# Kernel optimization log

Measured on AMD Instinct MI355X. Metric: run time of the kernel, lower is better.

The kernel has to match this reference:

```python
import jax, jax.numpy as jnp
import numpy as np

N, S_CT, D = 64, 128, 1024
WIN = 5
EPS = 1e-8
STOP = 0.1
MAX_DEPTH = 25


def layer_norm(x, g, b, eps=1e-5):
    mu = jnp.mean(x, axis=-1, keepdims=True)
    var = jnp.var(x, axis=-1, keepdims=True)
    return (x - mu) / jnp.sqrt(var + eps) * g + b


def _augment(sequence, input_mask, START, END):
    n, s, d = sequence.shape
    seq = jnp.concatenate([jnp.broadcast_to(START, (n, 1, d)), sequence], axis=1)
    m = jnp.concatenate([jnp.ones((n, 1, 1), seq.dtype), input_mask], axis=1)
    m_no_end = jnp.concatenate([m, jnp.zeros((n, 1, 1), seq.dtype)], axis=1)
    m_yes_end = jnp.concatenate([jnp.ones((n, 1, 1), seq.dtype), m], axis=1)
    end_mask = m_yes_end - m_no_end  # one-hot at END slot
    seq = jnp.concatenate([seq, jnp.zeros((n, 1, d), seq.dtype)], axis=1)
    seq = end_mask * END + (1.0 - end_mask) * seq
    m_no_start = jnp.concatenate([jnp.zeros((n, 1, 1), seq.dtype), m_yes_end[:, 1:]], axis=1)
    return seq, m_yes_end, end_mask, m_no_start, m_no_end


def _neighbor_probs(exist_probs, mask):
    # exist_probs, mask: (n,s,1). Returns left/right soft-neighbor matrices (n,s,s).
    n, s, _ = mask.shape
    m = jnp.stack([mask[:, ::-1, 0], mask[:, :, 0]], axis=1)            # (n,2,s)
    p = jnp.stack([exist_probs[:, ::-1, 0], exist_probs[:, :, 0]], axis=1)
    tri = jnp.triu(jnp.ones((s, s), mask.dtype), k=1)
    mat = (p * m)[:, :, None, :] * tri                                   # (n,2,s,s)
    cs = jnp.cumsum(mat, axis=-1)
    rem_left = jnp.concatenate([jnp.ones((n, 2, s, 1), mask.dtype), 1.0 - cs[..., :-1]], axis=-1)
    rem_left = jnp.maximum(rem_left, 0.0)
    right = jnp.where(cs > 1.0, rem_left, mat) * m[:, :, None, :]
    left = jnp.flip(right[:, 0], axis=(1, 2))
    return left, right[:, 1]


def crvnn_forward(sequence, input_mask, START, END, W_conv, b_conv, W_scorer, b_scorer,
                  W_init, b_init, W_cell1, b_cell1, W_cell2, b_cell2,
                  ln1_g, ln1_b, ln2_g, ln2_b):
    seq, mask, end_mask, m_no_start, m_no_end = _augment(sequence, input_mask, START, END)
    n, s, d = seq.shape
    last_mask = jnp.concatenate([end_mask[:, 1:], jnp.zeros((n, 1, 1), seq.dtype)], axis=1)
    sel_mask = m_no_start * m_no_end * (1.0 - last_mask)  # start_end_last_mask
    seq = layer_norm((seq * mask) @ W_init + b_init, ln1_g, ln1_b) * mask
    exist = jnp.ones((n, s, 1), seq.dtype) * mask

    def step(carry, _):
        sq, ep, um = carry
        L, R = _neighbor_probs(ep, mask)
        l1 = L @ sq; l2 = L @ l1
        r1 = R @ sq; r2 = R @ r1
        win = jnp.concatenate([l2, l1, sq, r1, r2], axis=-1)  # (n,s,5d) == stacked window flattened
        h = jax.nn.gelu(win @ W_conv + b_conv, approximate=False)
        sc = h @ W_scorer + b_scorer                           # (n,s,1) transition score
        scores = jnp.concatenate([sc, jnp.zeros_like(sc)], axis=-1)
        exp_scores = jnp.exp(scores - jnp.max(scores))
        exp_t = exp_scores[..., 0:1] * sel_mask
        exp_n = exp_scores[..., 1:2]
        # sum_normalize over {transition, no_op}; gate halted samples via um (tp=0 => no-op)
        tp = exp_t / (exp_t + exp_n + 2.0 * EPS) * um[:, None, None]
        # compose(left_child, self)
        cat = jnp.concatenate([l1, sq], axis=-1)
        hid = jax.nn.gelu(cat @ W_cell1 + b_cell1, approximate=False)
        contents = (hid @ W_cell2 + b_cell2).reshape(n, s, 4, d)
        gates = jax.nn.sigmoid(contents[:, :, 0:3, :])
        comp = layer_norm(gates[:, :, 0] * l1 + gates[:, :, 1] * sq + gates[:, :, 2] * contents[:, :, 3, :], ln2_g, ln2_b)
        new_sq = tp * comp + (1.0 - tp) * sq
        new_ep = ep * (1.0 - (R @ tp))  # left neighbor consumed with prob of right neighbor transition
        active = jnp.sum(new_ep * sel_mask, axis=(1, 2))
        new_um = um * (active >= STOP).astype(sq.dtype)
        return (new_sq, new_ep, new_um), None

    steps = min(s - 2, MAX_DEPTH)
    (seq, exist, _), _ = jax.lax.scan(step, (seq, exist, jnp.ones((n,), seq.dtype)), None, length=steps)
    seq = seq * mask
    global_state = jnp.sum(last_mask * seq, axis=1)  # root lands at last content slot
    return seq[:, 1:-1, :], global_state


def setup_inputs():
    key = jax.random.key(0)
    ks = jax.random.split(key, 8)
    sc = 0.02
    f32 = jnp.float32
    return {
        "sequence": jax.random.normal(ks[0], (N, S_CT, D), f32),
        "input_mask": jnp.ones((N, S_CT, 1), f32),
        "START": jax.random.normal(ks[1], (D,), f32),
        "END": jax.random.normal(ks[2], (D,), f32),
        "W_conv": jax.random.normal(ks[3], (WIN * D, D), f32) * sc,
        "b_conv": jnp.zeros((D,), f32),
        "W_scorer": jax.random.normal(ks[4], (D, 1), f32) * sc,
        "b_scorer": jnp.zeros((1,), f32),
        "W_init": jax.random.normal(ks[5], (D, D), f32) * sc,
        "b_init": jnp.zeros((D,), f32),
        "W_cell1": jax.random.normal(ks[6], (2 * D, 4 * D), f32) * sc,
        "b_cell1": jnp.zeros((4 * D,), f32),
        "W_cell2": jax.random.normal(ks[7], (4 * D, 4 * D), f32) * sc,
        "b_cell2": jnp.zeros((4 * D,), f32),
        "ln1_g": jnp.ones((D,), f32), "ln1_b": jnp.zeros((D,), f32),
        "ln2_g": jnp.ones((D,), f32), "ln2_b": jnp.zeros((D,), f32),
    }


def reference(sequence, input_mask, START, END, W_conv, b_conv, W_scorer, b_scorer,
              W_init, b_init, W_cell1, b_cell1, W_cell2, b_cell2,
              ln1_g, ln1_b, ln2_g, ln2_b):
    return crvnn_forward(sequence, input_mask, START, END, W_conv, b_conv, W_scorer, b_scorer,
                         W_init, b_init, W_cell1, b_cell1, W_cell2, b_cell2,
                         ln1_g, ln1_b, ln2_g, ln2_b)
```

## Files before the change

kernel.cpp:

```cpp
#include <hip/hip_runtime.h>
#include <math.h>


#define NB 64
#define SS 130
#define DD 1024
#define MM (NB*SS)
#define LSTR 132
#define CROWS 1664

typedef _Float16 f16x8 __attribute__((ext_vector_type(8)));
typedef _Float16 f16x4 __attribute__((ext_vector_type(4)));
typedef _Float16 f16x2 __attribute__((ext_vector_type(2)));
typedef float f32x4 __attribute__((ext_vector_type(4)));

struct GemmSrc { const float* a[5]; };

__device__ __forceinline__ float bsum(float v){
  __shared__ float sh[4];
  __syncthreads();
  #pragma unroll
  for (int o=32;o;o>>=1) v += __shfl_down(v,o);
  if ((threadIdx.x & 63)==0) sh[threadIdx.x>>6] = v;
  __syncthreads();
  return sh[0]+sh[1]+sh[2]+sh[3];
}
__device__ __forceinline__ float bmaxr(float v){
  __shared__ float sh[4];
  __syncthreads();
  #pragma unroll
  for (int o=32;o;o>>=1) v = fmaxf(v,__shfl_down(v,o));
  if ((threadIdx.x & 63)==0) sh[threadIdx.x>>6] = v;
  __syncthreads();
  return fmaxf(fmaxf(sh[0],sh[1]),fmaxf(sh[2],sh[3]));
}
__device__ __forceinline__ float gelu_(float x){
  return 0.5f*x*(1.f+erff(x*0.70710678118654752f));
}

__global__ __launch_bounds__(256) void build_masks(
    const float* __restrict__ im, float* __restrict__ mk, float* __restrict__ sel,
    float* __restrict__ lastm, float* __restrict__ endm, float* __restrict__ ep,
    float* __restrict__ um, int* __restrict__ flag){
  int b = blockIdx.x, i = threadIdx.x;
  if (i < SS){
    float mye = (i<=1) ? 1.f : im[b*128 + (i-2)];
    float mne = (i==SS-1) ? 0.f : ((i==0) ? 1.f : im[b*128 + (i-1)]);
    float em  = mye - mne;
    float mns = (i==0) ? 0.f : mye;
    float lm;
    if (i < SS-1){
      int i1 = i+1;
      float mye1 = (i1<=1) ? 1.f : im[b*128 + (i1-2)];
      float mne1 = (i1==SS-1) ? 0.f : im[b*128 + (i1-1)];
      lm = mye1 - mne1;
    } else lm = 0.f;
    float sl = mns * mne * (1.f - lm);
    int idx = b*SS + i;
    mk[idx]=mye; sel[idx]=sl; lastm[idx]=lm; endm[idx]=em; ep[idx]=mye;
  } else if (i == SS) { um[b] = 1.f; }
  else if (i == SS+1 && b==0) { flag[0] = 0; }
}

__global__ __launch_bounds__(256) void build_seq(
    const float* __restrict__ seqin, const float* __restrict__ START,
    const float* __restrict__ END, const float* __restrict__ mk,
    const float* __restrict__ endm, float* __restrict__ out){
  int r = blockIdx.x; int b = r/SS, i = r%SS; int t = threadIdx.x;
  float em = endm[r], m = mk[r];
  #pragma unroll
  for (int q=0;q<4;q++){
    int j = t + q*256;
    float v;
    if (i==0) v = START[j];
    else if (i<=128) v = seqin[((size_t)b*128 + (i-1))*DD + j];
    else v = 0.f;
    v = em*END[j] + (1.f-em)*v;
    out[(size_t)r*DD + j] = v*m;
  }
}

__global__ __launch_bounds__(256) void wtranspose(
    const float* __restrict__ W, _Float16* __restrict__ WTh, _Float16* __restrict__ WTl,
    int K, int N){
  __shared__ float Ts[32][33];
  int k0 = blockIdx.x*32, n0 = blockIdx.y*32;
  int t = threadIdx.x;
  int r = t>>3, c4 = (t&7)*4;
  float4 v = *(const float4*)(W + (size_t)(k0+r)*N + n0 + c4);
  Ts[r][c4]=v.x; Ts[r][c4+1]=v.y; Ts[r][c4+2]=v.z; Ts[r][c4+3]=v.w;
  __syncthreads();
  int n = t>>3, k4 = (t&7)*4;
  f16x4 h, lo;
  #pragma unroll
  for (int i=0;i<4;i++){
    float xs = Ts[k4+i][n] * 64.f;
    _Float16 hh = (_Float16)xs;
    h[i] = hh; lo[i] = (_Float16)((xs - (float)hh) * 2048.f);
  }
  *(f16x4*)(WTh + (size_t)(n0+n)*K + k0+k4) = h;
  *(f16x4*)(WTl + (size_t)(n0+n)*K + k0+k4) = lo;
}

template<bool PRE>
__global__ __launch_bounds__(256,2) void gemm_mfma(
    GemmSrc S, long lda,
    const _Float16* __restrict__ WTh, const _Float16* __restrict__ WTl,
    const float* __restrict__ Wf, int Nw,
    const float* __restrict__ bias,
    float* __restrict__ C, long ldc, int K, int act,
    const int* __restrict__ flag, float* __restrict__ spart, const float* __restrict__ Ws){
  if (flag[0]) return;
  __shared__ _Float16 Ah[128][40], Al[128][40];
  __shared__ _Float16 Wh[128][40], Wl[128][40];
  const int t = threadIdx.x;
  const int wave = t >> 6, lane = t & 63;
  const int wm = wave >> 1, wn = wave & 1;
  const int l15 = lane & 15, l4 = lane >> 4;
  const long mb = (long)blockIdx.y * 128;
  const int  nb = blockIdx.x * 128;
  f32x4 accH[4][4], accX[4][4];
  #pragma unroll
  for (int i=0;i<4;i++)
    #pragma unroll
    for (int j=0;j<4;j++){ accH[i][j] = (f32x4){0.f,0.f,0.f,0.f}; accX[i][j] = (f32x4){0.f,0.f,0.f,0.f}; }

  for (int kt=0; kt<K; kt+=32){
    #pragma unroll
    for (int p=0;p<4;p++){
      int f = t + 256*p;
      int m = f >> 3;
      int k4 = (f & 7) * 4;
      int kg = kt + k4;
      const float* src = S.a[kg >> 10];
      float4 v = *(const float4*)(src + (mb + m)*lda + (kg & 1023));
      f16x4 h, lo;
      _Float16 hh;
      hh=(_Float16)v.x; h[0]=hh; lo[0]=(_Float16)((v.x-(float)hh)*2048.f);
      hh=(_Float16)v.y; h[1]=hh; lo[1]=(_Float16)((v.y-(float)hh)*2048.f);
      hh=(_Float16)v.z; h[2]=hh; lo[2]=(_Float16)((v.z-(float)hh)*2048.f);
      hh=(_Float16)v.w; h[3]=hh; lo[3]=(_Float16)((v.w-(float)hh)*2048.f);
      *(f16x4*)&Ah[m][k4] = h;
      *(f16x4*)&Al[m][k4] = lo;
    }
    if constexpr (PRE){
      #pragma unroll
      for (int p=0;p<2;p++){
        int f = t + 256*p;
        int n = f >> 2;
        int ko = (f & 3) * 8;
        *(f16x8*)&Wh[n][ko] = *(const f16x8*)(WTh + (size_t)(nb + n)*K + kt + ko);
        *(f16x8*)&Wl[n][ko] = *(const f16x8*)(WTl + (size_t)(nb + n)*K + kt + ko);
      }
    } else {
      #pragma unroll
      for (int p=0;p<2;p++){
        int u = t + 256*p;
        int kp = u >> 5;
        int c  = u & 31;
        const float* wsrc = Wf + (size_t)(kt + 2*kp)*Nw + nb + c;
        #pragma unroll
        for (int i=0;i<4;i++){
          float x0 = wsrc[32*i] * 64.f;
          float x1 = wsrc[(size_t)Nw + 32*i] * 64.f;
          _Float16 h0 = (_Float16)x0, h1 = (_Float16)x1;
          _Float16 g0 = (_Float16)((x0 - (float)h0)*2048.f);
          _Float16 g1 = (_Float16)((x1 - (float)h1)*2048.f);
          f16x2 hp; hp[0]=h0; hp[1]=h1;
          f16x2 lp; lp[0]=g0; lp[1]=g1;
          int n = c + 32*i;
          *(f16x2*)&Wh[n][2*kp] = hp;
          *(f16x2*)&Wl[n][2*kp] = lp;
        }
      }
    }
    __syncthreads();
    f16x8 wh[4], wl[4];
    #pragma unroll
    for (int i=0;i<4;i++){
      wh[i] = *(const f16x8*)&Wh[wn*64 + i*16 + l15][8*l4];
      wl[i] = *(const f16x8*)&Wl[wn*64 + i*16 + l15][8*l4];
    }
    #pragma unroll
    for (int mi=0;mi<4;mi++){
      f16x8 ahv = *(const f16x8*)&Ah[wm*64 + mi*16 + l15][8*l4];
      f16x8 alv = *(const f16x8*)&Al[wm*64 + mi*16 + l15][8*l4];
      #pragma unroll
      for (int ni=0;ni<4;ni++){
        accH[mi][ni] = __builtin_amdgcn_mfma_f32_16x16x32_f16(wh[ni], ahv, accH[mi][ni], 0,0,0);
        accX[mi][ni] = __builtin_amdgcn_mfma_f32_16x16x32_f16(wh[ni], alv, accX[mi][ni], 0,0,0);
        accX[mi][ni] = __builtin_amdgcn_mfma_f32_16x16x32_f16(wl[ni], ahv, accX[mi][ni], 0,0,0);
      }
    }
    __syncthreads();
  }

  const float IH = 1.f/64.f, IX = 1.f/131072.f;
  if (act==2){
    #pragma unroll
    for (int mi=0;mi<4;mi++){
      float s = 0.f;
      #pragma unroll
      for (int ni=0;ni<4;ni++){
        int nbase = nb + wn*64 + ni*16 + 4*l4;
        #pragma unroll
        for (int r=0;r<4;r++){
          float v = gelu_(accH[mi][ni][r]*IH + accX[mi][ni][r]*IX + bias[nbase+r]);
          s = fmaf(v, Ws[nbase+r], s);
        }
      }
      s += __shfl_xor(s, 16);
      s += __shfl_xor(s, 32);
      if (l4==0){
        long m = mb + wm*64 + mi*16 + l15;
        spart[m*16 + blockIdx.x*2 + wn] = s;
      }
    }
    return;
  }
  #pragma unroll
  for (int mi=0;mi<4;mi++){
    long m = mb + wm*64 + mi*16 + l15;
    #pragma unroll
    for (int ni=0;ni<4;ni++){
      int nbase = nb + wn*64 + ni*16 + 4*l4;
      float4 v;
      v.x = accH[mi][ni][0]*IH + accX[mi][ni][0]*IX + bias[nbase+0];
      v.y = accH[mi][ni][1]*IH + accX[mi][ni][1]*IX + bias[nbase+1];
      v.z = accH[mi][ni][2]*IH + accX[mi][ni][2]*IX + bias[nbase+2];
      v.w = accH[mi][ni][3]*IH + accX[mi][ni][3]*IX + bias[nbase+3];
      if (act==1){ v.x=gelu_(v.x); v.y=gelu_(v.y); v.z=gelu_(v.z); v.w=gelu_(v.w); }
      *(float4*)(C + m*ldc + nbase) = v;
    }
  }
}

__global__ __launch_bounds__(256,2) void gemm_f32(
    GemmSrc S, long lda, const float* __restrict__ B, const float* __restrict__ bias,
    float* __restrict__ C, long ldc, int N, int K, int act,
    const int* __restrict__ flag){
  if (flag[0]) return;
  __shared__ float Asm[16][132];
  __shared__ float Bsm[16][132];
  float acc[8][8];
  #pragma unroll
  for (int i=0;i<8;i++)
    #pragma unroll
    for (int j=0;j<8;j++) acc[i][j]=0.f;
  const int t = threadIdx.x;
  const int tx = t & 15, ty = t >> 4;
  const long mb = (long)blockIdx.y * 128;
  const int  nb = blockIdx.x * 128;
  for (int kt=0; kt<K; kt+=16){
    #pragma unroll
    for (int ii=0; ii<2; ii++){
      int f  = t + 256*ii;
      int m  = f >> 2;
      int k4 = (f & 3) * 4;
      int kg = kt + k4;
      const float* src = S.a[kg >> 10];
      float4 v = *(const float4*)(src + (mb + m)*lda + (kg & 1023));
      Asm[k4+0][m]=v.x; Asm[k4+1][m]=v.y; Asm[k4+2][m]=v.z; Asm[k4+3][m]=v.w;
    }
    #pragma unroll
    for (int ii=0; ii<2; ii++){
      int f  = t + 256*ii;
      int kk = f >> 5;
      int c4 = (f & 31)*4;
      *(float4*)&Bsm[kk][c4] = *(const float4*)(B + (long)(kt+kk)*N + nb + c4);
    }
    __syncthreads();
    #pragma unroll
    for (int kk=0;kk<16;kk++){
      float av[8], bv[8];
      *(float4*)&av[0] = *(const float4*)&Asm[kk][ty*4];
      *(float4*)&av[4] = *(const float4*)&Asm[kk][64+ty*4];
      *(float4*)&bv[0] = *(const float4*)&Bsm[kk][tx*4];
      *(float4*)&bv[4] = *(const float4*)&Bsm[kk][64+tx*4];
      #pragma unroll
      for (int r=0;r<8;r++)
        #pragma unroll
        for (int c=0;c<8;c++) acc[r][c] = fmaf(av[r],bv[c],acc[r][c]);
    }
    __syncthreads();
  }
  #pragma unroll
  for (int rh=0;rh<2;rh++)
  #pragma unroll
  for (int rr=0;rr<4;rr++){
    long row = mb + rh*64 + ty*4 + rr;
    #pragma unroll
    for (int ch=0;ch<2;ch++){
      int col = nb + ch*64 + tx*4;
      float t0 = acc[rh*4+rr][ch*4+0] + bias[col+0];
      float t1 = acc[rh*4+rr][ch*4+1] + bias[col+1];
      float t2 = acc[rh*4+rr][ch*4+2] + bias[col+2];
      float t3 = acc[rh*4+rr][ch*4+3] + bias[col+3];
      if (act==1){ t0=gelu_(t0); t1=gelu_(t1); t2=gelu_(t2); t3=gelu_(t3); }
      float4 v; v.x=t0; v.y=t1; v.z=t2; v.w=t3;
      *(float4*)(C + row*ldc + col) = v;
    }
  }
}

__global__ __launch_bounds__(256,2) void bgemm(
    const float* __restrict__ P, const float* __restrict__ X, float* __restrict__ Y,
    const int* __restrict__ flag){
  if (flag[0]) return;
  __shared__ float Ps[64][17];
  __shared__ float Xs[16][132];
  const int t = threadIdx.x;
  const int nt = blockIdx.x, mt = blockIdx.y, b = blockIdx.z;
  const int i0 = mt*64;
  const float* Pb = P + (size_t)b*SS*LSTR;
  const float* Xb = X + (size_t)b*SS*DD + nt*128;
  float* Yb = Y + (size_t)b*SS*DD + nt*128;
  const int tx = t & 7, ty = t >> 3;
  float acc[2][16];
  #pragma unroll
  for (int r=0;r<2;r++)
    #pragma unroll
    for (int c=0;c<16;c++) acc[r][c]=0.f;
  for (int j0=0;j0<SS;j0+=16){
    { int r = t>>2, c0 = (t&3)*4;
      float4 v = make_float4(0.f,0.f,0.f,0.f);
      if (i0 + r < SS && j0 + c0 < LSTR) v = *(const float4*)(Pb + (size_t)(i0+r)*LSTR + j0 + c0);
      Ps[r][c0]=v.x; Ps[r][c0+1]=v.y; Ps[r][c0+2]=v.z; Ps[r][c0+3]=v.w;
    }
    #pragma unroll
    for (int ii=0;ii<2;ii++){
      int f = t + 256*ii;
      int jj = f>>5, c4 = (f&31)*4;
      float4 v = make_float4(0.f,0.f,0.f,0.f);
      if (j0 + jj < SS) v = *(const float4*)(Xb + (size_t)(j0+jj)*DD + c4);
      *(float4*)&Xs[jj][c4] = v;
    }
    __syncthreads();
    #pragma unroll
    for (int jj=0;jj<16;jj++){
      float p0 = Ps[2*ty][jj], p1 = Ps[2*ty+1][jj];
      #pragma unroll
      for (int q=0;q<4;q++){
        float4 xv = *(const float4*)&Xs[jj][tx*4 + 32*q];
        acc[0][q*4+0] = fmaf(p0,xv.x,acc[0][q*4+0]);
        acc[0][q*4+1] = fmaf(p0,xv.y,acc[0][q*4+1]);
        acc[0][q*4+2] = fmaf(p0,xv.z,acc[0][q*4+2]);
        acc[0][q*4+3] = fmaf(p0,xv.w,acc[0][q*4+3]);
        acc[1][q*4+0] = fmaf(p1,xv.x,acc[1][q*4+0]);
        acc[1][q*4+1] = fmaf(p1,xv.y,acc[1][q*4+1]);
        acc[1][q*4+2] = fmaf(p1,xv.z,acc[1][q*4+2]);
        acc[1][q*4+3] = fmaf(p1,xv.w,acc[1][q*4+3]);
      }
    }
    __syncthreads();
  }
  #pragma unroll
  for (int rr=0;rr<2;rr++){
    int row = i0 + 2*ty + rr;
    if (row < SS){
      #pragma unroll
      for (int q=0;q<4;q++){
        float4 v = make_float4(acc[rr][q*4],acc[rr][q*4+1],acc[rr][q*4+2],acc[rr][q*4+3]);
        *(float4*)(Yb + (size_t)row*DD + tx*4 + 32*q) = v;
      }
    }
  }
}

__global__ void neighbor_kernel(const float* __restrict__ ep, const float* __restrict__ mk,
                                float* __restrict__ L, float* __restrict__ R,
                                const int* __restrict__ flag){
  if (flag[0]) return;
  int idx = blockIdx.x*blockDim.x + threadIdx.x;
  if (idx >= MM) return;
  int b = idx / SS, i = idx % SS;
  const float* p = ep + b*SS;
  const float* m = mk + b*SS;
  float* Lr = L + (size_t)idx*LSTR;
  float* Rr = R + (size_t)idx*LSTR;
  for (int j=0;j<LSTR;j++){ Lr[j]=0.f; Rr[j]=0.f; }
  float cs=0.f;
  for (int j=i+1;j<SS;j++){
    float mat = p[j]*m[j];
    cs += mat;
    float v = (cs>1.f) ? fmaxf(1.f-(cs-mat),0.f) : mat;
    Rr[j] = v*m[j];
  }
  cs=0.f;
  for (int j=i-1;j>=0;j--){
    float mat = p[j]*m[j];
    cs += mat;
    float v = (cs>1.f) ? fmaxf(1.f-(cs-mat),0.f) : mat;
    Lr[j] = v*m[j];
  }
}

__global__ __launch_bounds__(256) void ln1_kernel(
    const float* __restrict__ xin, const float* __restrict__ g, const float* __restrict__ bb,
    const float* __restrict__ mk, float* __restrict__ out){
  int r = blockIdx.x, t = threadIdx.x;
  const float* xr = xin + (size_t)r*DD;
  float x[4]; float s=0.f;
  #pragma unroll
  for (int q=0;q<4;q++){ x[q]=xr[t+256*q]; s+=x[q]; }
  float mean = bsum(s)*(1.f/DD);
  float vs=0.f;
  #pragma unroll
  for (int q=0;q<4;q++){ float d=x[q]-mean; vs+=d*d; }
  float var = bsum(vs)*(1.f/DD);
  float inv = 1.f/sqrtf(var+1e-5f);
  float m = mk[r];
  #pragma unroll
  for (int q=0;q<4;q++){ int j=t+256*q; out[(size_t)r*DD+j] = ((x[q]-mean)*inv*g[j]+bb[j])*m; }
}

__global__ void scorer_final(const float* __restrict__ spart, const float* __restrict__ bs,
                             float* __restrict__ sc, const int* __restrict__ flag){
  if (flag[0]) return;
  int r = blockIdx.x*blockDim.x + threadIdx.x;
  if (r >= MM) return;
  float s = bs[0];
  #pragma unroll
  for (int k=0;k<16;k++) s += spart[(size_t)r*16+k];
  sc[r] = s;
}
__global__ __launch_bounds__(256) void max1(const float* __restrict__ sc, float* __restrict__ part,
                                            const int* __restrict__ flag){
  if (flag[0]) return;
  int idx = blockIdx.x*256 + threadIdx.x;
  float v = -1e30f;
  for (int i = idx; i < MM; i += 64*256) v = fmaxf(v, sc[i]);
  v = bmaxr(v);
  if (threadIdx.x==0) part[blockIdx.x] = v;
}
__global__ __launch_bounds__(64) void max2(const float* __restrict__ part, float* __restrict__ gm,
                                           const int* __restrict__ flag){
  if (flag[0]) return;
  float v = part[threadIdx.x];
  #pragma unroll
  for (int o=32;o;o>>=1) v = fmaxf(v, __shfl_down(v,o));
  if (threadIdx.x==0) gm[0] = fmaxf(v, 0.f);
}
__global__ void tp_kernel(const float* __restrict__ sc, const float* __restrict__ sel,
                          const float* __restrict__ um, const float* __restrict__ gm,
                          float* __restrict__ tp, const int* __restrict__ flag){
  if (flag[0]) return;
  int idx = blockIdx.x*blockDim.x + threadIdx.x;
  if (idx>=MM) return;
  int b = idx / SS;
  float g = gm[0];
  float et = expf(sc[idx]-g)*sel[idx];
  float en = expf(-g);
  tp[idx] = et/(et+en+2e-8f)*um[b];
}

__global__ __launch_bounds__(256) void update_kernel(
    const float* __restrict__ cont, const float* __restrict__ l1, float* __restrict__ sq,
    const float* __restrict__ tp, const float* __restrict__ g, const float* __restrict__ bb,
    const int* __restrict__ flag, long row0){
  if (flag[0]) return;
  long r = row0 + blockIdx.x; int t = threadIdx.x;
  const float* cr = cont + (size_t)blockIdx.x*4096;
  const float* lr = l1 + (size_t)r*DD;
  float* sr = sq + (size_t)r*DD;
  float x[4], sv[4];
  float s=0.f;
  #pragma unroll
  for (int q=0;q<4;q++){
    int j = t+q*256;
    float c0=cr[j], c1=cr[DD+j], c2=cr[2*DD+j], c3=cr[3*DD+j];
    float g0=1.f/(1.f+expf(-c0));
    float g1=1.f/(1.f+expf(-c1));
    float g2=1.f/(1.f+expf(-c2));
    float lv=lr[j]; float sqv=sr[j]; sv[q]=sqv;
    x[q] = g0*lv + g1*sqv + g2*c3;
    s += x[q];
  }
  float mean = bsum(s)*(1.f/DD);
  float vs=0.f;
  #pragma unroll
  for (int q=0;q<4;q++){ float d=x[q]-mean; vs+=d*d; }
  float var = bsum(vs)*(1.f/DD);
  float inv = 1.f/sqrtf(var+1e-5f);
  float tpv = tp[r];
  #pragma unroll
  for (int q=0;q<4;q++){
    int j=t+q*256;
    float comp = (x[q]-mean)*inv*g[j]+bb[j];
    sr[j] = tpv*comp + (1.f-tpv)*sv[q];
  }
}

__global__ void ep_update(float* __restrict__ ep, const float* __restrict__ R,
                          const float* __restrict__ tp, const int* __restrict__ flag){
  if (flag[0]) return;
  int idx = blockIdx.x*blockDim.x + threadIdx.x;
  if (idx>=MM) return;
  int b = idx / SS;
  const float* Rr = R + (size_t)idx*LSTR;
  const float* tb = tp + b*SS;
  float d=0.f;
  for (int j=0;j<SS;j++) d = fmaf(Rr[j],tb[j],d);
  ep[idx] *= (1.f - d);
}
__global__ __launch_bounds__(256) void active_um(const float* __restrict__ ep,
                                                 const float* __restrict__ sel,
                                                 float* __restrict__ um,
                                                 const int* __restrict__ flag){
  if (flag[0]) return;
  int b = blockIdx.x, t = threadIdx.x;
  float s = (t<SS) ? ep[b*SS+t]*sel[b*SS+t] : 0.f;
  s = bsum(s);
  if (t==0) um[b] *= (s >= 0.1f) ? 1.f : 0.f;
}
__global__ __launch_bounds__(64) void done_kernel(const float* __restrict__ um, int* __restrict__ flag){
  float v = um[threadIdx.x];
  unsigned long long b = __ballot(v > 0.f);
  if (threadIdx.x==0) flag[0] = (b==0ULL) ? 1 : 0;
}

__global__ __launch_bounds__(256) void output_kernel(const float* __restrict__ sq,
                                                     const float* __restrict__ mk,
                                                     float* __restrict__ out){
  int r = blockIdx.x; int b = r/SS, i = r%SS;
  if (i<1 || i>128) return;
  float m = mk[r]; int t=threadIdx.x;
  #pragma unroll
  for (int q=0;q<4;q++){
    int j = t+q*256;
    out[((size_t)b*128 + (i-1))*DD + j] = sq[(size_t)r*DD + j]*m;
  }
}
__global__ __launch_bounds__(256) void gstate_kernel(const float* __restrict__ sq,
                                                     const float* __restrict__ mk,
                                                     const float* __restrict__ lastm,
                                                     float* __restrict__ outg){
  int b = blockIdx.x; int t=threadIdx.x;
  #pragma unroll
  for (int q=0;q<4;q++){
    int j = t+q*256;
    float acc=0.f;
    for (int i=0;i<SS;i++){
      float w = lastm[b*SS+i]*mk[b*SS+i];
      acc = fmaf(w, sq[((size_t)(b*SS+i))*DD + j], acc);
    }
    outg[(size_t)b*DD + j] = acc;
  }
}

extern "C" void kernel_launch(void* const* d_in, const int* in_sizes, int n_in,
                              void* d_out, int out_size, void* d_ws, size_t ws_size,
                              hipStream_t stream) {
  const float* sequence   = (const float*)d_in[0];
  const float* input_mask = (const float*)d_in[1];
  const float* START      = (const float*)d_in[2];
  const float* END        = (const float*)d_in[3];
  const float* W_conv     = (const float*)d_in[4];
  const float* b_conv     = (const float*)d_in[5];
  const float* W_scorer   = (const float*)d_in[6];
  const float* b_scorer   = (const float*)d_in[7];
  const float* W_init     = (const float*)d_in[8];
  const float* b_init     = (const float*)d_in[9];
  const float* W_cell1    = (const float*)d_in[10];
  const float* b_cell1    = (const float*)d_in[11];
  const float* W_cell2    = (const float*)d_in[12];
  const float* b_cell2    = (const float*)d_in[13];
  const float* ln1g       = (const float*)d_in[14];
  const float* ln1b       = (const float*)d_in[15];
  const float* ln2g       = (const float*)d_in[16];
  const float* ln2b       = (const float*)d_in[17];

  float* ws = (float*)d_ws;
  const size_t U = (size_t)MM*DD;
  float* sq   = ws;
  float* l1   = ws + U;
  float* r1   = ws + 2*U;
  float* l2   = ws + 3*U;
  float* r2   = ws + 4*U;
  float* Lm   = ws + 5*U;
  float* Rm   = Lm + (size_t)NB*SS*LSTR;
  float* maskv= Rm + (size_t)NB*SS*LSTR;
  float* sel  = maskv + MM;
  float* lastm= sel + MM;
  float* endm = lastm + MM;
  float* ep   = endm + MM;
  float* scb  = ep + MM;
  float* tpb  = scb + MM;
  float* spart= tpb + MM;
  float* umb  = spart + (size_t)MM*16;
  float* part = umb + NB;
  float* gmx  = part + 64;
  int*   flag = (int*)(gmx + 4);
  size_t used_floats = (size_t)((float*)(flag+4) - ws);
  used_floats = (used_floats + 7) & ~(size_t)7;
  _Float16* WTc_h = (_Float16*)(ws + used_floats);
  const size_t SC = (size_t)1024*5120, S1 = (size_t)4096*2048, S2 = (size_t)4096*4096;
  _Float16* WTc_l = WTc_h + SC;
  _Float16* WT1_h = WTc_l + SC;
  _Float16* WT1_l = WT1_h + S1;
  _Float16* WT2_h = WT1_l + S1;
  _Float16* WT2_l = WT2_h + S2;
  size_t need_pre = (size_t)((char*)(WT2_l + S2) - (char*)d_ws);
  const bool pre = ws_size >= need_pre;

  build_masks<<<NB,256,0,stream>>>(input_mask, maskv, sel, lastm, endm, ep, umb, flag);
  build_seq<<<MM,256,0,stream>>>(sequence, START, END, maskv, endm, r1);
  GemmSrc si; si.a[0]=r1; si.a[1]=r1; si.a[2]=r1; si.a[3]=r1; si.a[4]=r1;
  gemm_f32<<<dim3(8,65),256,0,stream>>>(si, DD, W_init, b_init, l2, DD, DD, DD, 0, flag);
  ln1_kernel<<<MM,256,0,stream>>>(l2, ln1g, ln1b, maskv, sq);

  if (pre){
    wtranspose<<<dim3(160,32),256,0,stream>>>(W_conv,  WTc_h, WTc_l, 5120, 1024);
    wtranspose<<<dim3(64,128),256,0,stream>>>(W_cell1, WT1_h, WT1_l, 2048, 4096);
    wtranspose<<<dim3(128,128),256,0,stream>>>(W_cell2, WT2_h, WT2_l, 4096, 4096);
  }

  for (int it=0; it<25; ++it){
    neighbor_kernel<<<(MM+255)/256,256,0,stream>>>(ep, maskv, Lm, Rm, flag);
    bgemm<<<dim3(8,3,NB),256,0,stream>>>(Lm, sq, l1, flag);
    bgemm<<<dim3(8,3,NB),256,0,stream>>>(Rm, sq, r1, flag);
    bgemm<<<dim3(8,3,NB),256,0,stream>>>(Lm, l1, l2, flag);
    bgemm<<<dim3(8,3,NB),256,0,stream>>>(Rm, r1, r2, flag);
    GemmSrc s5; s5.a[0]=l2; s5.a[1]=l1; s5.a[2]=sq; s5.a[3]=r1; s5.a[4]=r2;
    if (pre)
      gemm_mfma<true ><<<dim3(8,65),256,0,stream>>>(s5, DD, WTc_h, WTc_l, nullptr, 0, b_conv, nullptr, 0, 5120, 2, flag, spart, W_scorer);
    else
      gemm_mfma<false><<<dim3(8,65),256,0,stream>>>(s5, DD, nullptr, nullptr, W_conv, 1024, b_conv, nullptr, 0, 5120, 2, flag, spart, W_scorer);
    scorer_final<<<(MM+255)/256,256,0,stream>>>(spart, b_scorer, scb, flag);
    max1<<<64,256,0,stream>>>(scb, part, flag);
    max2<<<1,64,0,stream>>>(part, gmx, flag);
    tp_kernel<<<(MM+255)/256,256,0,stream>>>(scb, sel, umb, gmx, tpb, flag);
    for (int c=0;c<5;c++){
      long row0 = (long)c*CROWS;
      GemmSrc s2; s2.a[0]=l1+row0*DD; s2.a[1]=sq+row0*DD; s2.a[2]=s2.a[1]; s2.a[3]=s2.a[1]; s2.a[4]=s2.a[1];
      GemmSrc s3; s3.a[0]=l2; s3.a[1]=l2+DD; s3.a[2]=l2+2*DD; s3.a[3]=l2+3*DD; s3.a[4]=l2;
      if (pre){
        gemm_mfma<true ><<<dim3(32,13),256,0,stream>>>(s2, DD,   WT1_h, WT1_l, nullptr, 0, b_cell1, l2, 4096, 2048, 1, flag, nullptr, nullptr);
        gemm_mfma<true ><<<dim3(32,13),256,0,stream>>>(s3, 4096, WT2_h, WT2_l, nullptr, 0, b_cell2, r2, 4096, 4096, 0, flag, nullptr, nullptr);
      } else {
        gemm_mfma<false><<<dim3(32,13),256,0,stream>>>(s2, DD,   nullptr, nullptr, W_cell1, 4096, b_cell1, l2, 4096, 2048, 1, flag, nullptr, nullptr);
        gemm_mfma<false><<<dim3(32,13),256,0,stream>>>(s3, 4096, nullptr, nullptr, W_cell2, 4096, b_cell2, r2, 4096, 4096, 0, flag, nullptr, nullptr);
      }
      update_kernel<<<CROWS,256,0,stream>>>(r2, l1, sq, tpb, ln2g, ln2b, flag, row0);
    }
    ep_update<<<(MM+255)/256,256,0,stream>>>(ep, Rm, tpb, flag);
    active_um<<<NB,256,0,stream>>>(ep, sel, umb, flag);
    done_kernel<<<1,64,0,stream>>>(umb, flag);
  }

  float* out = (float*)d_out;
  output_kernel<<<MM,256,0,stream>>>(sq, maskv, out);
  gstate_kernel<<<NB,256,0,stream>>>(sq, maskv, lastm, out + (size_t)NB*128*DD);
}
```

Measured before the change: 68.64 ms.

## Widen MFMA GEMM tiles to 128x256 with 512 threads and XCD-aware block remap

```diff
diff --git a/kernel.cpp b/kernel.cpp
--- a/kernel.cpp
+++ b/kernel.cpp
@@ -103,7 +103,7 @@
 }
 
 template<bool PRE>
-__global__ __launch_bounds__(256,2) void gemm_mfma(
+__global__ __launch_bounds__(512,2) void gemm_mfma(
     GemmSrc S, long lda,
     const _Float16* __restrict__ WTh, const _Float16* __restrict__ WTl,
     const float* __restrict__ Wf, int Nw,
@@ -112,13 +112,20 @@
     const int* __restrict__ flag, float* __restrict__ spart, const float* __restrict__ Ws){
   if (flag[0]) return;
   __shared__ _Float16 Ah[128][40], Al[128][40];
-  __shared__ _Float16 Wh[128][40], Wl[128][40];
+  __shared__ _Float16 Wh[256][40], Wl[256][40];
   const int t = threadIdx.x;
   const int wave = t >> 6, lane = t & 63;
-  const int wm = wave >> 1, wn = wave & 1;
+  const int wm = wave >> 2, wn = wave & 3;
   const int l15 = lane & 15, l4 = lane >> 4;
-  const long mb = (long)blockIdx.y * 128;
-  const int  nb = blockIdx.x * 128;
+  int lin = blockIdx.y * gridDim.x + blockIdx.x;
+  int nwg = gridDim.x * gridDim.y;
+  int q = nwg >> 3, r = nwg & 7;
+  int xcd = lin & 7, pos = lin >> 3;
+  int wg = (xcd < r) ? (xcd*(q+1) + pos) : (r*(q+1) + (xcd - r)*q + pos);
+  int MT = gridDim.y;
+  int mt = wg % MT, nt = wg / MT;
+  const long mb = (long)mt * 128;
+  const int  nb = nt * 256;
   f32x4 accH[4][4], accX[4][4];
   #pragma unroll
   for (int i=0;i<4;i++)
@@ -127,8 +134,8 @@
 
   for (int kt=0; kt<K; kt+=32){
     #pragma unroll
-    for (int p=0;p<4;p++){
-      int f = t + 256*p;
+    for (int p=0;p<2;p++){
+      int f = t + 512*p;
       int m = f >> 3;
       int k4 = (f & 7) * 4;
       int kg = kt + k4;
@@ -146,32 +153,28 @@
     if constexpr (PRE){
       #pragma unroll
       for (int p=0;p<2;p++){
-        int f = t + 256*p;
+        int f = t + 512*p;
         int n = f >> 2;
         int ko = (f & 3) * 8;
         *(f16x8*)&Wh[n][ko] = *(const f16x8*)(WTh + (size_t)(nb + n)*K + kt + ko);
         *(f16x8*)&Wl[n][ko] = *(const f16x8*)(WTl + (size_t)(nb + n)*K + kt + ko);
       }
     } else {
+      int kp = t >> 5;
+      int c  = t & 31;
+      const float* wsrc = Wf + (size_t)(kt + 2*kp)*Nw + nb + c;
       #pragma unroll
-      for (int p=0;p<2;p++){
-        int u = t + 256*p;
-        int kp = u >> 5;
-        int c  = u & 31;
-        const float* wsrc = Wf + (size_t)(kt + 2*kp)*Nw + nb + c;
-        #pragma unroll
-        for (int i=0;i<4;i++){
-          float x0 = wsrc[32*i] * 64.f;
-          float x1 = wsrc[(size_t)Nw + 32*i] * 64.f;
-          _Float16 h0 = (_Float16)x0, h1 = (_Float16)x1;
-          _Float16 g0 = (_Float16)((x0 - (float)h0)*2048.f);
-          _Float16 g1 = (_Float16)((x1 - (float)h1)*2048.f);
-          f16x2 hp; hp[0]=h0; hp[1]=h1;
-          f16x2 lp; lp[0]=g0; lp[1]=g1;
-          int n = c + 32*i;
-          *(f16x2*)&Wh[n][2*kp] = hp;
-          *(f16x2*)&Wl[n][2*kp] = lp;
-        }
+      for (int i=0;i<8;i++){
+        float x0 = wsrc[32*i] * 64.f;
+        float x1 = wsrc[(size_t)Nw + 32*i] * 64.f;
+        _Float16 h0 = (_Float16)x0, h1 = (_Float16)x1;
+        _Float16 g0 = (_Float16)((x0 - (float)h0)*2048.f);
+        _Float16 g1 = (_Float16)((x1 - (float)h1)*2048.f);
+        f16x2 hp; hp[0]=h0; hp[1]=h1;
+        f16x2 lp; lp[0]=g0; lp[1]=g1;
+        int n = c + 32*i;
+        *(f16x2*)&Wh[n][2*kp] = hp;
+        *(f16x2*)&Wl[n][2*kp] = lp;
       }
     }
     __syncthreads();
@@ -204,16 +207,16 @@
       for (int ni=0;ni<4;ni++){
         int nbase = nb + wn*64 + ni*16 + 4*l4;
         #pragma unroll
-        for (int r=0;r<4;r++){
-          float v = gelu_(accH[mi][ni][r]*IH + accX[mi][ni][r]*IX + bias[nbase+r]);
-          s = fmaf(v, Ws[nbase+r], s);
+        for (int rr=0;rr<4;rr++){
+          float v = gelu_(accH[mi][ni][rr]*IH + accX[mi][ni][rr]*IX + bias[nbase+rr]);
+          s = fmaf(v, Ws[nbase+rr], s);
         }
       }
       s += __shfl_xor(s, 16);
       s += __shfl_xor(s, 32);
       if (l4==0){
         long m = mb + wm*64 + mi*16 + l15;
-        spart[m*16 + blockIdx.x*2 + wn] = s;
+        spart[m*16 + nt*4 + wn] = s;
       }
     }
     return;
@@ -593,15 +596,16 @@
   int*   flag = (int*)(gmx + 4);
   size_t used_floats = (size_t)((float*)(flag+4) - ws);
   used_floats = (used_floats + 7) & ~(size_t)7;
-  _Float16* WTc_h = (_Float16*)(ws + used_floats);
   const size_t SC = (size_t)1024*5120, S1 = (size_t)4096*2048, S2 = (size_t)4096*4096;
+  _Float16* WT2_h = (_Float16*)(ws + used_floats);
+  _Float16* WT2_l = WT2_h + S2;
+  _Float16* WT1_h = WT2_l + S2;
+  _Float16* WT1_l = WT1_h + S1;
+  _Float16* WTc_h = WT1_l + S1;
   _Float16* WTc_l = WTc_h + SC;
-  _Float16* WT1_h = WTc_l + SC;
-  _Float16* WT1_l = WT1_h + S1;
-  _Float16* WT2_h = WT1_l + S1;
-  _Float16* WT2_l = WT2_h + S2;
-  size_t need_pre = (size_t)((char*)(WT2_l + S2) - (char*)d_ws);
-  const bool pre = ws_size >= need_pre;
+  const bool pre2 = ws_size >= (size_t)((char*)(WT2_l + S2) - (char*)d_ws);
+  const bool pre1 = ws_size >= (size_t)((char*)(WT1_l + S1) - (char*)d_ws);
+  const bool prec = ws_size >= (size_t)((char*)(WTc_l + SC) - (char*)d_ws);
 
   build_masks<<<NB,256,0,stream>>>(input_mask, maskv, sel, lastm, endm, ep, umb, flag);
   build_seq<<<MM,256,0,stream>>>(sequence, START, END, maskv, endm, r1);
@@ -609,11 +613,9 @@
   gemm_f32<<<dim3(8,65),256,0,stream>>>(si, DD, W_init, b_init, l2, DD, DD, DD, 0, flag);
   ln1_kernel<<<MM,256,0,stream>>>(l2, ln1g, ln1b, maskv, sq);
 
-  if (pre){
-    wtranspose<<<dim3(160,32),256,0,stream>>>(W_conv,  WTc_h, WTc_l, 5120, 1024);
-    wtranspose<<<dim3(64,128),256,0,stream>>>(W_cell1, WT1_h, WT1_l, 2048, 4096);
-    wtranspose<<<dim3(128,128),256,0,stream>>>(W_cell2, WT2_h, WT2_l, 4096, 4096);
-  }
+  if (pre2) wtranspose<<<dim3(128,128),256,0,stream>>>(W_cell2, WT2_h, WT2_l, 4096, 4096);
+  if (pre1) wtranspose<<<dim3(64,128),256,0,stream>>>(W_cell1, WT1_h, WT1_l, 2048, 4096);
+  if (prec) wtranspose<<<dim3(160,32),256,0,stream>>>(W_conv,  WTc_h, WTc_l, 5120, 1024);
 
   for (int it=0; it<25; ++it){
     neighbor_kernel<<<(MM+255)/256,256,0,stream>>>(ep, maskv, Lm, Rm, flag);
@@ -622,10 +624,10 @@
     bgemm<<<dim3(8,3,NB),256,0,stream>>>(Lm, l1, l2, flag);
     bgemm<<<dim3(8,3,NB),256,0,stream>>>(Rm, r1, r2, flag);
     GemmSrc s5; s5.a[0]=l2; s5.a[1]=l1; s5.a[2]=sq; s5.a[3]=r1; s5.a[4]=r2;
-    if (pre)
-      gemm_mfma<true ><<<dim3(8,65),256,0,stream>>>(s5, DD, WTc_h, WTc_l, nullptr, 0, b_conv, nullptr, 0, 5120, 2, flag, spart, W_scorer);
+    if (prec)
+      gemm_mfma<true ><<<dim3(4,65),512,0,stream>>>(s5, DD, WTc_h, WTc_l, nullptr, 0, b_conv, nullptr, 0, 5120, 2, flag, spart, W_scorer);
     else
-      gemm_mfma<false><<<dim3(8,65),256,0,stream>>>(s5, DD, nullptr, nullptr, W_conv, 1024, b_conv, nullptr, 0, 5120, 2, flag, spart, W_scorer);
+      gemm_mfma<false><<<dim3(4,65),512,0,stream>>>(s5, DD, nullptr, nullptr, W_conv, 1024, b_conv, nullptr, 0, 5120, 2, flag, spart, W_scorer);
     scorer_final<<<(MM+255)/256,256,0,stream>>>(spart, b_scorer, scb, flag);
     max1<<<64,256,0,stream>>>(scb, part, flag);
     max2<<<1,64,0,stream>>>(part, gmx, flag);
@@ -634,13 +636,14 @@
       long row0 = (long)c*CROWS;
       GemmSrc s2; s2.a[0]=l1+row0*DD; s2.a[1]=sq+row0*DD; s2.a[2]=s2.a[1]; s2.a[3]=s2.a[1]; s2.a[4]=s2.a[1];
       GemmSrc s3; s3.a[0]=l2; s3.a[1]=l2+DD; s3.a[2]=l2+2*DD; s3.a[3]=l2+3*DD; s3.a[4]=l2;
-      if (pre){
-        gemm_mfma<true ><<<dim3(32,13),256,0,stream>>>(s2, DD,   WT1_h, WT1_l, nullptr, 0, b_cell1, l2, 4096, 2048, 1, flag, nullptr, nullptr);
-        gemm_mfma<true ><<<dim3(32,13),256,0,stream>>>(s3, 4096, WT2_h, WT2_l, nullptr, 0, b_cell2, r2, 4096, 4096, 0, flag, nullptr, nullptr);
-      } else {
-        gemm_mfma<false><<<dim3(32,13),256,0,stream>>>(s2, DD,   nullptr, nullptr, W_cell1, 4096, b_cell1, l2, 4096, 2048, 1, flag, nullptr, nullptr);
-        gemm_mfma<false><<<dim3(32,13),256,0,stream>>>(s3, 4096, nullptr, nullptr, W_cell2, 4096, b_cell2, r2, 4096, 4096, 0, flag, nullptr, nullptr);
-      }
+      if (pre1)
+        gemm_mfma<true ><<<dim3(16,13),512,0,stream>>>(s2, DD,   WT1_h, WT1_l, nullptr, 0, b_cell1, l2, 4096, 2048, 1, flag, nullptr, nullptr);
+      else
+        gemm_mfma<false><<<dim3(16,13),512,0,stream>>>(s2, DD,   nullptr, nullptr, W_cell1, 4096, b_cell1, l2, 4096, 2048, 1, flag, nullptr, nullptr);
+      if (pre2)
+        gemm_mfma<true ><<<dim3(16,13),512,0,stream>>>(s3, 4096, WT2_h, WT2_l, nullptr, 0, b_cell2, r2, 4096, 4096, 0, flag, nullptr, nullptr);
+      else
+        gemm_mfma<false><<<dim3(16,13),512,0,stream>>>(s3, 4096, nullptr, nullptr, W_cell2, 4096, b_cell2, r2, 4096, 4096, 0, flag, nullptr, nullptr);
       update_kernel<<<CROWS,256,0,stream>>>(r2, l1, sq, tpb, ln2g, ln2b, flag, row0);
     }
     ep_update<<<(MM+255)/256,256,0,stream>>>(ep, Rm, tpb, flag);
```

Result: slower. 79.19 ms (+15.4%).
